# Kernel tuning notes

Hardware: AMD Instinct MI355X
Metric: run time of the kernel (lower is better)

The kernel has to match this reference:

```python
import jax, jax.numpy as jnp
import numpy as np

B, S, D, H = 2, 2048, 1024, 16
DH = D // H  # head dim = 64


def setup_inputs() -> dict:
    key = jax.random.key(0)
    ks = jax.random.split(key, 10)
    q = jax.random.normal(ks[0], (B, S, D), dtype=jnp.float32)
    k = jax.random.normal(ks[1], (B, S, D), dtype=jnp.float32)
    v = jax.random.normal(ks[2], (B, S, D), dtype=jnp.float32)
    # causal mask: True = masked (as in masked_fill)
    causal = jnp.triu(jnp.ones((S, S), dtype=bool), k=1)
    mask = jnp.broadcast_to(causal, (B, S, S))
    sc = 1.0 / np.sqrt(D)
    Wv = jax.random.normal(ks[3], (DH, D), dtype=jnp.float32) * sc
    bv = jnp.zeros((DH,), dtype=jnp.float32)
    Wq = jax.random.normal(ks[4], (H, DH, D), dtype=jnp.float32) * sc  # per-head query proj
    bq = jnp.zeros((H, DH), dtype=jnp.float32)
    Wk = jax.random.normal(ks[5], (H, DH, D), dtype=jnp.float32) * sc  # per-head key proj
    bk = jnp.zeros((H, DH), dtype=jnp.float32)
    Wo = jax.random.normal(ks[6], (D, DH), dtype=jnp.float32) * (1.0 / np.sqrt(DH))  # final proj, no bias
    return {"q": q, "k": k, "v": v, "mask": mask,
            "Wv": Wv, "bv": bv, "Wq": Wq, "bq": bq, "Wk": Wk, "bk": bk, "Wo": Wo}


def reference(q, k, v, mask, Wv, bv, Wq, bq, Wk, bk, Wo):
    # shared value projection across heads: [B,S,DH]
    v_proj = jnp.einsum('bsd,ed->bse', v, Wv) + bv
    # per-head Q/K projections, batched over heads: [B,H,S,DH]
    qh = jnp.einsum('bsd,hed->bhse', q, Wq) + bq[None, :, None, :]
    kh = jnp.einsum('bsd,hed->bhse', k, Wk) + bk[None, :, None, :]
    scale = jnp.sqrt(jnp.asarray(DH, dtype=qh.dtype))
    attn = jnp.einsum('bhse,bhte->bhst', qh, kh) / scale  # [B,H,S,S]
    attn = jnp.where(mask[:, None, :, :], jnp.asarray(-1e9, attn.dtype), attn)
    attn = jax.nn.softmax(attn, axis=-1)
    out_h = jnp.einsum('bhst,bte->bhse', attn, v_proj)  # shared V across heads
    mean_head = out_h.mean(axis=1)  # mean over heads: [B,S,DH]
    out = jnp.einsum('bse,de->bsd', mean_head, Wo)  # [B,S,D]
    attn_stacked = jnp.transpose(attn, (0, 2, 1, 3))  # [B,S,H,S] to match torch.stack(dim=2)
    return out, attn_stacked
```

## Files before the change

### kernel.cpp

```cpp
#include <hip/hip_runtime.h>
#include <cstdint>
#include <math.h>

typedef unsigned short u16;
typedef __bf16 bf16x8 __attribute__((ext_vector_type(8)));
typedef float f32x4 __attribute__((ext_vector_type(4)));

constexpr int Bc = 2, Sc = 2048, Dc = 1024, Hc = 16, DHc = 64;

__device__ __forceinline__ u16 f2bf(float f) {
  uint32_t u = __builtin_bit_cast(uint32_t, f);
  u += 0x7fffu + ((u >> 16) & 1u);
  return (u16)(u >> 16);
}
__device__ __forceinline__ float bf2f(u16 h) {
  uint32_t u = ((uint32_t)h) << 16;
  return __builtin_bit_cast(float, u);
}
__device__ __forceinline__ f32x4 mfma16(bf16x8 a, bf16x8 b, f32x4 c) {
  return __builtin_amdgcn_mfma_f32_16x16x32_bf16(a, b, c, 0, 0, 0);
}
__device__ __forceinline__ void gload16(const void* g, void* l) {
  __builtin_amdgcn_global_load_lds((const uint32_t*)g, (uint32_t*)l, 16, 0, 0);
}
__device__ __forceinline__ bf16x8 pk8(f32x4 a, f32x4 b) {
  alignas(16) u16 t[8];
  #pragma unroll
  for (int j = 0; j < 4; ++j) { t[j] = f2bf(a[j]); t[4 + j] = f2bf(b[j]); }
  return *reinterpret_cast<const bf16x8*>(t);
}

__global__ __launch_bounds__(256) void cvt_all(
    const float* __restrict__ q, const float* __restrict__ k, const float* __restrict__ v,
    const float* __restrict__ Wq, const float* __restrict__ Wk,
    const float* __restrict__ Wv, const float* __restrict__ Wo,
    u16* __restrict__ qo, u16* __restrict__ ko, u16* __restrict__ vo,
    u16* __restrict__ Wqo, u16* __restrict__ Wko, u16* __restrict__ Wvo,
    u16* __restrict__ Woo) {
  constexpr int NQ = Bc * Sc * Dc / 4;
  constexpr int NW = Hc * DHc * Dc / 4;
  constexpr int NS = DHc * Dc / 4;
  constexpr int C1 = NQ, C2 = 2 * NQ, C3 = 3 * NQ;
  constexpr int C4 = C3 + NW, C5 = C4 + NW, C6 = C5 + NS, C7 = C6 + NS;
  const int i = blockIdx.x * 256 + threadIdx.x;
  if (i >= C7) return;
  const float* src; u16* dst; int j;
  if (i < C1)      { src = q;  dst = qo;  j = i; }
  else if (i < C2) { src = k;  dst = ko;  j = i - C1; }
  else if (i < C3) { src = v;  dst = vo;  j = i - C2; }
  else if (i < C4) { src = Wq; dst = Wqo; j = i - C3; }
  else if (i < C5) { src = Wk; dst = Wko; j = i - C4; }
  else if (i < C6) { src = Wv; dst = Wvo; j = i - C5; }
  else             { src = Wo; dst = Woo; j = i - C6; }
  float4 x = reinterpret_cast<const float4*>(src)[j];
  ushort4 o;
  o.x = f2bf(x.x); o.y = f2bf(x.y); o.z = f2bf(x.z); o.w = f2bf(x.w);
  reinterpret_cast<ushort4*>(dst)[j] = o;
}

__global__ __launch_bounds__(256) void gemm_qkv(
    const u16* __restrict__ qbf, const u16* __restrict__ kbf, const u16* __restrict__ vbf,
    const u16* __restrict__ Wqb, const u16* __restrict__ Wkb, const u16* __restrict__ Wvb,
    const float* __restrict__ bq, const float* __restrict__ bk, const float* __restrict__ bv,
    float qscale, u16* __restrict__ qh, u16* __restrict__ kh, u16* __restrict__ vT) {
  constexpr int K = 1024;
  const int z = blockIdx.z;
  if (z == 2 && blockIdx.x != 0) return;
  const u16* A  = z == 0 ? qbf : (z == 1 ? kbf : vbf);
  const u16* Bw = z == 0 ? Wqb : (z == 1 ? Wkb : Wvb);
  const float* bias = z == 0 ? bq : (z == 1 ? bk : bv);
  const float scale = z == 0 ? qscale : 1.0f;

  __shared__ u16 As[128 * 32];
  __shared__ u16 Bs[128 * 32];
  const int tid = threadIdx.x;
  const int lane = tid & 63;
  const int w = tid >> 6, wm = w >> 1, wn = w & 1;
  const int lo = lane & 15, hi = lane >> 4;
  const int m0 = blockIdx.y * 128, n0 = blockIdx.x * 128;
  const int r16 = lane >> 2;
  const int c8 = (lane & 3) * 8;
  const f32x4 vzero = {0.f, 0.f, 0.f, 0.f};

  f32x4 acc[4][4];
  #pragma unroll
  for (int i = 0; i < 4; ++i)
    #pragma unroll
    for (int j = 0; j < 4; ++j) acc[i][j] = vzero;

  for (int k0 = 0; k0 < K; k0 += 32) {
    #pragma unroll
    for (int it = 0; it < 2; ++it) {
      const int rg = w * 2 + it;
      const int row = rg * 16 + r16;
      gload16(&A[(long)(m0 + row) * K + k0 + c8], &As[rg * 512]);
      gload16(&Bw[(long)(n0 + row) * K + k0 + c8], &Bs[rg * 512]);
    }
    __syncthreads();
    bf16x8 af[4], bfr[4];
    #pragma unroll
    for (int mi = 0; mi < 4; ++mi)
      af[mi] = *reinterpret_cast<const bf16x8*>(&As[(wm * 64 + mi * 16 + lo) * 32 + hi * 8]);
    #pragma unroll
    for (int nj = 0; nj < 4; ++nj)
      bfr[nj] = *reinterpret_cast<const bf16x8*>(&Bs[(wn * 64 + nj * 16 + lo) * 32 + hi * 8]);
    #pragma unroll
    for (int mi = 0; mi < 4; ++mi)
      #pragma unroll
      for (int nj = 0; nj < 4; ++nj)
        acc[mi][nj] = mfma16(af[mi], bfr[nj], acc[mi][nj]);
    __syncthreads();
  }

  #pragma unroll
  for (int nj = 0; nj < 4; ++nj) {
    const int n = n0 + wn * 64 + nj * 16 + lo;
    if (z == 2 && n >= 64) continue;
    const float bb = bias[n];
    #pragma unroll
    for (int mi = 0; mi < 4; ++mi) {
      #pragma unroll
      for (int r = 0; r < 4; ++r) {
        const int mm = m0 + wm * 64 + mi * 16 + hi * 4 + r;
        const int bidx = mm >> 11, ss = mm & 2047;
        const float val = (acc[mi][nj][r] + bb) * scale;
        if (z < 2) {
          const int hh = n >> 6, ee = n & 63;
          const long idx = bidx * 2097152L + ss * 64L + hh * 131072L + ee;
          (z ? kh : qh)[idx] = f2bf(val);
        } else {
          vT[bidx * 131072L + n * 2048L + ss] = f2bf(val);
        }
      }
    }
  }
}

__global__ __launch_bounds__(256) void gemm_bt(
    const u16* __restrict__ A, const u16* __restrict__ Bw,
    const float* __restrict__ bias, int M, int N, int K, float scale,
    u16* __restrict__ outb, float* __restrict__ outf,
    int DHn, long strideB, long strideS, long strideH, long strideE) {
  __shared__ u16 As[128 * 32];
  __shared__ u16 Bs[128 * 32];
  const int tid = threadIdx.x;
  const int lane = tid & 63;
  const int w = tid >> 6, wm = w >> 1, wn = w & 1;
  const int lo = lane & 15, hi = lane >> 4;
  const int m0 = blockIdx.y * 128, n0 = blockIdx.x * 128;
  const int r16 = lane >> 2;
  const int c8 = (lane & 3) * 8;
  const f32x4 vzero = {0.f, 0.f, 0.f, 0.f};

  f32x4 acc[4][4];
  #pragma unroll
  for (int i = 0; i < 4; ++i)
    #pragma unroll
    for (int j = 0; j < 4; ++j) acc[i][j] = vzero;

  for (int k0 = 0; k0 < K; k0 += 32) {
    #pragma unroll
    for (int it = 0; it < 2; ++it) {
      const int rg = w * 2 + it;
      const int row = rg * 16 + r16;
      gload16(&A[(long)(m0 + row) * K + k0 + c8], &As[rg * 512]);
      gload16(&Bw[(long)(n0 + row) * K + k0 + c8], &Bs[rg * 512]);
    }
    __syncthreads();
    bf16x8 af[4], bfr[4];
    #pragma unroll
    for (int mi = 0; mi < 4; ++mi)
      af[mi] = *reinterpret_cast<const bf16x8*>(&As[(wm * 64 + mi * 16 + lo) * 32 + hi * 8]);
    #pragma unroll
    for (int nj = 0; nj < 4; ++nj)
      bfr[nj] = *reinterpret_cast<const bf16x8*>(&Bs[(wn * 64 + nj * 16 + lo) * 32 + hi * 8]);
    #pragma unroll
    for (int mi = 0; mi < 4; ++mi)
      #pragma unroll
      for (int nj = 0; nj < 4; ++nj)
        acc[mi][nj] = mfma16(af[mi], bfr[nj], acc[mi][nj]);
    __syncthreads();
  }

  #pragma unroll
  for (int nj = 0; nj < 4; ++nj) {
    const int n = n0 + wn * 64 + nj * 16 + lo;
    if (n >= N) continue;
    const float bb = bias ? bias[n] : 0.f;
    const int hh = n / DHn, ee = n % DHn;
    #pragma unroll
    for (int mi = 0; mi < 4; ++mi) {
      #pragma unroll
      for (int r = 0; r < 4; ++r) {
        const int mm = m0 + wm * 64 + mi * 16 + hi * 4 + r;
        const int bidx = mm >> 11, ss = mm & 2047;
        const long idx = bidx * strideB + ss * strideS + hh * strideH + ee * strideE;
        const float val = (acc[mi][nj][r] + bb) * scale;
        if (outf) outf[idx] = val;
        else outb[idx] = f2bf(val);
      }
    }
  }
}

__global__ __launch_bounds__(256) void attn_fused(
    const u16* __restrict__ qh, const u16* __restrict__ kh,
    const u16* __restrict__ vT, u16* __restrict__ outh,
    float* __restrict__ attn_out) {
  __shared__ float pslds[4][16][68];
  __shared__ float pofflds[4][16];
  const int tid = threadIdx.x;
  const int lane = tid & 63, w = tid >> 6;
  const int lo = lane & 15, hi = lane >> 4;
  const int blk = blockIdx.x;
  const int sb = blk & 15, h = (blk >> 4) & 15, b = blk >> 8;
  const long bh = (long)(b * Hc + h) * Sc;
  const long rowstride = (long)Hc * Sc;
  float* aout = attn_out + (long)b * Sc * rowstride + (long)h * Sc;
  float (*pf)[68] = pslds[w];
  float* poff = pofflds[w];
  const f32x4 vzero = {0.f, 0.f, 0.f, 0.f};
  const int idx = sb * 4 + w;
  const float M0 = 16.f;

  #pragma unroll 1
  for (int sp = 0; sp < 2; ++sp) {
    const int strip = sp ? 127 - idx : idx;
    const int s0 = strip * 16;
    const int smax = s0 + 15;
    const int send = (smax / 64 + 1) * 64;
    const int srow = s0 + hi * 4;
    const int srow2 = s0 + lo;

    bf16x8 qa0, qa1;
    {
      const u16* qp = &qh[(bh + s0 + lo) * DHc];
      qa0 = *reinterpret_cast<const bf16x8*>(&qp[hi * 8]);
      qa1 = *reinterpret_cast<const bf16x8*>(&qp[32 + hi * 8]);
    }

    float lr[4];
    #pragma unroll
    for (int r = 0; r < 4; ++r) lr[r] = 0.f;

    for (int t0 = 0; t0 < send; t0 += 64) {
      f32x4 z[4];
      #pragma unroll
      for (int c = 0; c < 4; ++c) {
        const u16* kp = &kh[(bh + t0 + c * 16 + lo) * DHc];
        bf16x8 kb0 = *reinterpret_cast<const bf16x8*>(&kp[hi * 8]);
        bf16x8 kb1 = *reinterpret_cast<const bf16x8*>(&kp[32 + hi * 8]);
        f32x4 zz = mfma16(qa0, kb0, vzero);
        z[c] = mfma16(qa1, kb1, zz);
      }
      const bool full = (t0 + 63 <= s0);
      #pragma unroll
      for (int r = 0; r < 4; ++r) {
        const int s = srow + r;
        #pragma unroll
        for (int c = 0; c < 4; ++c) {
          float e = exp2f(z[c][r] - M0);
          if (!full) e = ((t0 + c * 16 + lo) <= s) ? e : 0.f;
          lr[r] += e;
        }
      }
    }
    #pragma unroll
    for (int r = 0; r < 4; ++r) {
      #pragma unroll
      for (int dd = 1; dd < 16; dd <<= 1) lr[r] += __shfl_xor(lr[r], dd);
    }
    if (lo == 0) {
      #pragma unroll
      for (int r = 0; r < 4; ++r) poff[hi * 4 + r] = M0 + __log2f(lr[r]);
    }
    asm volatile("s_waitcnt lgkmcnt(0)" ::: "memory");
    __builtin_amdgcn_sched_barrier(0);
    const float offv = poff[lo];

    f32x4 acco[4];
    #pragma unroll
    for (int eb = 0; eb < 4; ++eb) acco[eb] = vzero;
    const int r4 = lane >> 4;
    const int c4 = (lane & 15) * 4;
    for (int t0 = 0; t0 < send; t0 += 64) {
      const bool full = (t0 + 63 <= s0);
      #pragma unroll
      for (int c = 0; c < 4; ++c) {
        const u16* kp = &kh[(bh + t0 + c * 16 + lo) * DHc];
        bf16x8 kb0 = *reinterpret_cast<const bf16x8*>(&kp[hi * 8]);
        bf16x8 kb1 = *reinterpret_cast<const bf16x8*>(&kp[32 + hi * 8]);
        f32x4 zt = mfma16(kb1, qa1, mfma16(kb0, qa0, vzero));
        f32x4 p;
        #pragma unroll
        for (int r = 0; r < 4; ++r) {
          const float e = exp2f(zt[r] - offv);
          p[r] = (full || (t0 + c * 16 + hi * 4 + r <= srow2)) ? e : 0.f;
        }
        *reinterpret_cast<f32x4*>(&pf[lo][c * 16 + hi * 4]) = p;
      }
      asm volatile("s_waitcnt lgkmcnt(0)" ::: "memory");
      __builtin_amdgcn_sched_barrier(0);
      #pragma unroll
      for (int j = 0; j < 4; ++j) {
        f32x4 v = *reinterpret_cast<const f32x4*>(&pf[j * 4 + r4][c4]);
        __builtin_nontemporal_store(
            v, reinterpret_cast<f32x4*>(aout + (long)(s0 + j * 4 + r4) * rowstride + t0 + c4));
      }
      f32x4 a0 = *reinterpret_cast<const f32x4*>(&pf[lo][hi * 8]);
      f32x4 a1 = *reinterpret_cast<const f32x4*>(&pf[lo][hi * 8 + 4]);
      f32x4 a2 = *reinterpret_cast<const f32x4*>(&pf[lo][32 + hi * 8]);
      f32x4 a3 = *reinterpret_cast<const f32x4*>(&pf[lo][32 + hi * 8 + 4]);
      bf16x8 pa0 = pk8(a0, a1);
      bf16x8 pa1 = pk8(a2, a3);
      const u16* vp = &vT[((long)b * DHc + lo) * Sc + t0 + hi * 8];
      #pragma unroll
      for (int eb = 0; eb < 4; ++eb) {
        bf16x8 vb0 = *reinterpret_cast<const bf16x8*>(&vp[(long)eb * 16 * Sc]);
        bf16x8 vb1 = *reinterpret_cast<const bf16x8*>(&vp[(long)eb * 16 * Sc + 32]);
        acco[eb] = mfma16(pa0, vb0, acco[eb]);
        acco[eb] = mfma16(pa1, vb1, acco[eb]);
      }
    }

    #pragma unroll
    for (int eb = 0; eb < 4; ++eb)
      #pragma unroll
      for (int r = 0; r < 4; ++r)
        outh[(bh + srow + r) * DHc + eb * 16 + lo] = f2bf(acco[eb][r]);

    const f32x4 z4 = {0.f, 0.f, 0.f, 0.f};
    for (int t0 = send; t0 < Sc; t0 += 64) {
      #pragma unroll
      for (int r = 0; r < 4; ++r)
        __builtin_nontemporal_store(
            z4, reinterpret_cast<f32x4*>(aout + (long)(srow + r) * rowstride + t0 + lo * 4));
    }
  }
}

__global__ __launch_bounds__(256) void mean_kernel(const u16* __restrict__ outh,
                                                   u16* __restrict__ meanb) {
  const int idx = blockIdx.x * 256 + threadIdx.x;
  const int bs = idx >> 3;
  const int e0 = (idx & 7) * 8;
  const int b = bs >> 11, s = bs & 2047;
  float acc[8];
  #pragma unroll
  for (int j = 0; j < 8; ++j) acc[j] = 0.f;
  for (int h = 0; h < Hc; ++h) {
    alignas(16) u16 tmp[8];
    *reinterpret_cast<uint4*>(tmp) =
        *reinterpret_cast<const uint4*>(&outh[((long)(b * Hc + h) * Sc + s) * DHc + e0]);
    #pragma unroll
    for (int j = 0; j < 8; ++j) acc[j] += bf2f(tmp[j]);
  }
  alignas(16) u16 o[8];
  #pragma unroll
  for (int j = 0; j < 8; ++j) o[j] = f2bf(acc[j] * 0.0625f);
  *reinterpret_cast<uint4*>(&meanb[(long)bs * DHc + e0]) = *reinterpret_cast<const uint4*>(o);
}

extern "C" void kernel_launch(void* const* d_in, const int* in_sizes, int n_in,
                              void* d_out, int out_size, void* d_ws, size_t ws_size,
                              hipStream_t stream) {
  (void)in_sizes; (void)n_in; (void)out_size; (void)ws_size;
  const float* q  = (const float*)d_in[0];
  const float* k  = (const float*)d_in[1];
  const float* v  = (const float*)d_in[2];
  const float* Wv = (const float*)d_in[4];
  const float* bv = (const float*)d_in[5];
  const float* Wq = (const float*)d_in[6];
  const float* bq = (const float*)d_in[7];
  const float* Wk = (const float*)d_in[8];
  const float* bk = (const float*)d_in[9];
  const float* Wo = (const float*)d_in[10];

  char* ws = (char*)d_ws;
  u16* qbf   = (u16*)(ws + 0);
  u16* kbf   = (u16*)(ws + 8388608);
  u16* vbf   = (u16*)(ws + 16777216);
  u16* Wqbf  = (u16*)(ws + 25165824);
  u16* Wkbf  = (u16*)(ws + 27262976);
  u16* Wvbf  = (u16*)(ws + 29360128);
  u16* Wobf  = (u16*)(ws + 29491200);
  u16* qhb   = (u16*)(ws + 29622272);
  u16* khb   = (u16*)(ws + 38010880);
  u16* vTb   = (u16*)(ws + 46399488);
  u16* outh  = (u16*)(ws + 46923776);
  u16* meanb = (u16*)(ws + 55312384);

  float* outp  = (float*)d_out;
  float* attnp = (float*)d_out + (long)Bc * Sc * Dc;

  cvt_all<<<(3702784 + 255) / 256, 256, 0, stream>>>(
      q, k, v, Wq, Wk, Wv, Wo, qbf, kbf, vbf, Wqbf, Wkbf, Wvbf, Wobf);

  const int M = Bc * Sc;
  const float qscale = 0.125f * 1.4426950408889634f;
  gemm_qkv<<<dim3(8, 32, 3), 256, 0, stream>>>(
      qbf, kbf, vbf, Wqbf, Wkbf, Wvbf, bq, bk, bv, qscale, qhb, khb, vTb);

  attn_fused<<<512, 256, 0, stream>>>(qhb, khb, vTb, outh, attnp);

  mean_kernel<<<128, 256, 0, stream>>>(outh, meanb);

  gemm_bt<<<dim3(8, 32), 256, 0, stream>>>(meanb, Wobf, nullptr, M, 1024, 64, 1.0f,
      nullptr, outp, 1024, 2097152L, 1024L, 0L, 1L);
}
```

Measured before the change: 267.4 us.

## Process both causal strips together per wave to share K and V loads

Each wave used to handle its short and long query strips one after the other. It now runs both strips interleaved in a single pair of passes over the keys, so every K tile and V tile loaded from memory serves both strips whenever the short strip is still active. This removes roughly a third of the K/V global loads and the second loop's setup overhead, and adds independent MFMA work to hide latency. The cost is double the LDS scratch and more live registers (two sets of Q fragments, accumulators and K/V fragments), which may reduce occupancy.

```diff
diff --git a/kernel.cpp b/kernel.cpp
--- a/kernel.cpp
+++ b/kernel.cpp
@@ -207,8 +207,8 @@
     const u16* __restrict__ qh, const u16* __restrict__ kh,
     const u16* __restrict__ vT, u16* __restrict__ outh,
     float* __restrict__ attn_out) {
-  __shared__ float pslds[4][16][68];
-  __shared__ float pofflds[4][16];
+  __shared__ float pslds[2][4][16][68];
+  __shared__ float pofflds[2][4][16];
   const int tid = threadIdx.x;
   const int lane = tid & 63, w = tid >> 6;
   const int lo = lane & 15, hi = lane >> 4;
@@ -217,125 +217,203 @@
   const long bh = (long)(b * Hc + h) * Sc;
   const long rowstride = (long)Hc * Sc;
   float* aout = attn_out + (long)b * Sc * rowstride + (long)h * Sc;
-  float (*pf)[68] = pslds[w];
-  float* poff = pofflds[w];
+  float (*pfA)[68] = pslds[0][w];
+  float (*pfB)[68] = pslds[1][w];
+  float* poffA = pofflds[0][w];
+  float* poffB = pofflds[1][w];
   const f32x4 vzero = {0.f, 0.f, 0.f, 0.f};
   const int idx = sb * 4 + w;
   const float M0 = 16.f;
 
-  #pragma unroll 1
-  for (int sp = 0; sp < 2; ++sp) {
-    const int strip = sp ? 127 - idx : idx;
-    const int s0 = strip * 16;
-    const int smax = s0 + 15;
-    const int send = (smax / 64 + 1) * 64;
-    const int srow = s0 + hi * 4;
-    const int srow2 = s0 + lo;
-
-    bf16x8 qa0, qa1;
+  const int s0A = idx * 16;
+  const int s0B = (127 - idx) * 16;
+  const int sendA = (s0A + 79) & ~63;
+  const int sendB = (s0B + 79) & ~63;
+  const int srowA = s0A + hi * 4;
+  const int srowB = s0B + hi * 4;
+  const int srow2A = s0A + lo;
+  const int srow2B = s0B + lo;
+
+  bf16x8 qaA0, qaA1, qaB0, qaB1;
+  {
+    const u16* qpA = &qh[(bh + s0A + lo) * DHc];
+    qaA0 = *reinterpret_cast<const bf16x8*>(&qpA[hi * 8]);
+    qaA1 = *reinterpret_cast<const bf16x8*>(&qpA[32 + hi * 8]);
+    const u16* qpB = &qh[(bh + s0B + lo) * DHc];
+    qaB0 = *reinterpret_cast<const bf16x8*>(&qpB[hi * 8]);
+    qaB1 = *reinterpret_cast<const bf16x8*>(&qpB[32 + hi * 8]);
+  }
+
+  float lrA[4], lrB[4];
+  #pragma unroll
+  for (int r = 0; r < 4; ++r) { lrA[r] = 0.f; lrB[r] = 0.f; }
+
+  for (int t0 = 0; t0 < sendB; t0 += 64) {
+    bf16x8 kb[4][2];
+    #pragma unroll
+    for (int c = 0; c < 4; ++c) {
+      const u16* kp = &kh[(bh + t0 + c * 16 + lo) * DHc];
+      kb[c][0] = *reinterpret_cast<const bf16x8*>(&kp[hi * 8]);
+      kb[c][1] = *reinterpret_cast<const bf16x8*>(&kp[32 + hi * 8]);
+    }
+    const bool doA = (t0 < sendA);
     {
-      const u16* qp = &qh[(bh + s0 + lo) * DHc];
-      qa0 = *reinterpret_cast<const bf16x8*>(&qp[hi * 8]);
-      qa1 = *reinterpret_cast<const bf16x8*>(&qp[32 + hi * 8]);
-    }
-
-    float lr[4];
-    #pragma unroll
-    for (int r = 0; r < 4; ++r) lr[r] = 0.f;
-
-    for (int t0 = 0; t0 < send; t0 += 64) {
-      f32x4 z[4];
+      const bool fullB = (t0 + 63 <= s0B);
       #pragma unroll
       for (int c = 0; c < 4; ++c) {
-        const u16* kp = &kh[(bh + t0 + c * 16 + lo) * DHc];
-        bf16x8 kb0 = *reinterpret_cast<const bf16x8*>(&kp[hi * 8]);
-        bf16x8 kb1 = *reinterpret_cast<const bf16x8*>(&kp[32 + hi * 8]);
-        f32x4 zz = mfma16(qa0, kb0, vzero);
-        z[c] = mfma16(qa1, kb1, zz);
-      }
-      const bool full = (t0 + 63 <= s0);
-      #pragma unroll
-      for (int r = 0; r < 4; ++r) {
-        const int s = srow + r;
+        f32x4 z = mfma16(qaB1, kb[c][1], mfma16(qaB0, kb[c][0], vzero));
         #pragma unroll
-        for (int c = 0; c < 4; ++c) {
-          float e = exp2f(z[c][r] - M0);
-          if (!full) e = ((t0 + c * 16 + lo) <= s) ? e : 0.f;
-          lr[r] += e;
+        for (int r = 0; r < 4; ++r) {
+          float e = exp2f(z[r] - M0);
+          if (!fullB) e = ((t0 + c * 16 + lo) <= srowB + r) ? e : 0.f;
+          lrB[r] += e;
         }
       }
     }
+    if (doA) {
+      const bool fullA = (t0 + 63 <= s0A);
+      #pragma unroll
+      for (int c = 0; c < 4; ++c) {
+        f32x4 z = mfma16(qaA1, kb[c][1], mfma16(qaA0, kb[c][0], vzero));
+        #pragma unroll
+        for (int r = 0; r < 4; ++r) {
+          float e = exp2f(z[r] - M0);
+          if (!fullA) e = ((t0 + c * 16 + lo) <= srowA + r) ? e : 0.f;
+          lrA[r] += e;
+        }
+      }
+    }
+  }
+  #pragma unroll
+  for (int r = 0; r < 4; ++r) {
+    #pragma unroll
+    for (int dd = 1; dd < 16; dd <<= 1) {
+      lrA[r] += __shfl_xor(lrA[r], dd);
+      lrB[r] += __shfl_xor(lrB[r], dd);
+    }
+  }
+  if (lo == 0) {
     #pragma unroll
     for (int r = 0; r < 4; ++r) {
-      #pragma unroll
-      for (int dd = 1; dd < 16; dd <<= 1) lr[r] += __shfl_xor(lr[r], dd);
-    }
-    if (lo == 0) {
-      #pragma unroll
-      for (int r = 0; r < 4; ++r) poff[hi * 4 + r] = M0 + __log2f(lr[r]);
-    }
-    asm volatile("s_waitcnt lgkmcnt(0)" ::: "memory");
-    __builtin_amdgcn_sched_barrier(0);
-    const float offv = poff[lo];
-
-    f32x4 acco[4];
-    #pragma unroll
-    for (int eb = 0; eb < 4; ++eb) acco[eb] = vzero;
-    const int r4 = lane >> 4;
-    const int c4 = (lane & 15) * 4;
-    for (int t0 = 0; t0 < send; t0 += 64) {
-      const bool full = (t0 + 63 <= s0);
+      poffA[hi * 4 + r] = M0 + __log2f(lrA[r]);
+      poffB[hi * 4 + r] = M0 + __log2f(lrB[r]);
+    }
+  }
+  asm volatile("s_waitcnt lgkmcnt(0)" ::: "memory");
+  __builtin_amdgcn_sched_barrier(0);
+  const float offA = poffA[lo];
+  const float offB = poffB[lo];
+
+  f32x4 accoA[4], accoB[4];
+  #pragma unroll
+  for (int eb = 0; eb < 4; ++eb) { accoA[eb] = vzero; accoB[eb] = vzero; }
+  const int r4 = lane >> 4;
+  const int c4 = (lane & 15) * 4;
+
+  for (int t0 = 0; t0 < sendB; t0 += 64) {
+    bf16x8 kb[4][2];
+    #pragma unroll
+    for (int c = 0; c < 4; ++c) {
+      const u16* kp = &kh[(bh + t0 + c * 16 + lo) * DHc];
+      kb[c][0] = *reinterpret_cast<const bf16x8*>(&kp[hi * 8]);
+      kb[c][1] = *reinterpret_cast<const bf16x8*>(&kp[32 + hi * 8]);
+    }
+    const bool doA = (t0 < sendA);
+    {
+      const bool fullB = (t0 + 63 <= s0B);
       #pragma unroll
       for (int c = 0; c < 4; ++c) {
-        const u16* kp = &kh[(bh + t0 + c * 16 + lo) * DHc];
-        bf16x8 kb0 = *reinterpret_cast<const bf16x8*>(&kp[hi * 8]);
-        bf16x8 kb1 = *reinterpret_cast<const bf16x8*>(&kp[32 + hi * 8]);
-        f32x4 zt = mfma16(kb1, qa1, mfma16(kb0, qa0, vzero));
+        f32x4 zt = mfma16(kb[c][1], qaB1, mfma16(kb[c][0], qaB0, vzero));
         f32x4 p;
         #pragma unroll
         for (int r = 0; r < 4; ++r) {
-          const float e = exp2f(zt[r] - offv);
-          p[r] = (full || (t0 + c * 16 + hi * 4 + r <= srow2)) ? e : 0.f;
+          const float e = exp2f(zt[r] - offB);
+          p[r] = (fullB || (t0 + c * 16 + hi * 4 + r <= srow2B)) ? e : 0.f;
         }
-        *reinterpret_cast<f32x4*>(&pf[lo][c * 16 + hi * 4]) = p;
-      }
-      asm volatile("s_waitcnt lgkmcnt(0)" ::: "memory");
-      __builtin_amdgcn_sched_barrier(0);
+        *reinterpret_cast<f32x4*>(&pfB[lo][c * 16 + hi * 4]) = p;
+      }
+    }
+    if (doA) {
+      const bool fullA = (t0 + 63 <= s0A);
+      #pragma unroll
+      for (int c = 0; c < 4; ++c) {
+        f32x4 zt = mfma16(kb[c][1], qaA1, mfma16(kb[c][0], qaA0, vzero));
+        f32x4 p;
+        #pragma unroll
+        for (int r = 0; r < 4; ++r) {
+          const float e = exp2f(zt[r] - offA);
+          p[r] = (fullA || (t0 + c * 16 + hi * 4 + r <= srow2A)) ? e : 0.f;
+        }
+        *reinterpret_cast<f32x4*>(&pfA[lo][c * 16 + hi * 4]) = p;
+      }
+    }
+    asm volatile("s_waitcnt lgkmcnt(0)" ::: "memory");
+    __builtin_amdgcn_sched_barrier(0);
+    #pragma unroll
+    for (int j = 0; j < 4; ++j) {
+      f32x4 v = *reinterpret_cast<const f32x4*>(&pfB[j * 4 + r4][c4]);
+      __builtin_nontemporal_store(
+          v, reinterpret_cast<f32x4*>(aout + (long)(s0B + j * 4 + r4) * rowstride + t0 + c4));
+    }
+    if (doA) {
       #pragma unroll
       for (int j = 0; j < 4; ++j) {
-        f32x4 v = *reinterpret_cast<const f32x4*>(&pf[j * 4 + r4][c4]);
+        f32x4 v = *reinterpret_cast<const f32x4*>(&pfA[j * 4 + r4][c4]);
         __builtin_nontemporal_store(
-            v, reinterpret_cast<f32x4*>(aout + (long)(s0 + j * 4 + r4) * rowstride + t0 + c4));
-      }
-      f32x4 a0 = *reinterpret_cast<const f32x4*>(&pf[lo][hi * 8]);
-      f32x4 a1 = *reinterpret_cast<const f32x4*>(&pf[lo][hi * 8 + 4]);
-      f32x4 a2 = *reinterpret_cast<const f32x4*>(&pf[lo][32 + hi * 8]);
-      f32x4 a3 = *reinterpret_cast<const f32x4*>(&pf[lo][32 + hi * 8 + 4]);
+            v, reinterpret_cast<f32x4*>(aout + (long)(s0A + j * 4 + r4) * rowstride + t0 + c4));
+      }
+    }
+    bf16x8 vb[4][2];
+    const u16* vp = &vT[((long)b * DHc + lo) * Sc + t0 + hi * 8];
+    #pragma unroll
+    for (int eb = 0; eb < 4; ++eb) {
+      vb[eb][0] = *reinterpret_cast<const bf16x8*>(&vp[(long)eb * 16 * Sc]);
+      vb[eb][1] = *reinterpret_cast<const bf16x8*>(&vp[(long)eb * 16 * Sc + 32]);
+    }
+    {
+      f32x4 a0 = *reinterpret_cast<const f32x4*>(&pfB[lo][hi * 8]);
+      f32x4 a1 = *reinterpret_cast<const f32x4*>(&pfB[lo][hi * 8 + 4]);
+      f32x4 a2 = *reinterpret_cast<const f32x4*>(&pfB[lo][32 + hi * 8]);
+      f32x4 a3 = *reinterpret_cast<const f32x4*>(&pfB[lo][32 + hi * 8 + 4]);
       bf16x8 pa0 = pk8(a0, a1);
       bf16x8 pa1 = pk8(a2, a3);
-      const u16* vp = &vT[((long)b * DHc + lo) * Sc + t0 + hi * 8];
-      #pragma unroll
-      for (int eb = 0; eb < 4; ++eb) {
-        bf16x8 vb0 = *reinterpret_cast<const bf16x8*>(&vp[(long)eb * 16 * Sc]);
-        bf16x8 vb1 = *reinterpret_cast<const bf16x8*>(&vp[(long)eb * 16 * Sc + 32]);
-        acco[eb] = mfma16(pa0, vb0, acco[eb]);
-        acco[eb] = mfma16(pa1, vb1, acco[eb]);
-      }
-    }
-
-    #pragma unroll
-    for (int eb = 0; eb < 4; ++eb)
-      #pragma unroll
-      for (int r = 0; r < 4; ++r)
-        outh[(bh + srow + r) * DHc + eb * 16 + lo] = f2bf(acco[eb][r]);
-
-    const f32x4 z4 = {0.f, 0.f, 0.f, 0.f};
-    for (int t0 = send; t0 < Sc; t0 += 64) {
-      #pragma unroll
-      for (int r = 0; r < 4; ++r)
-        __builtin_nontemporal_store(
-            z4, reinterpret_cast<f32x4*>(aout + (long)(srow + r) * rowstride + t0 + lo * 4));
-    }
+      #pragma unroll
+      for (int eb = 0; eb < 4; ++eb)
+        accoB[eb] = mfma16(pa1, vb[eb][1], mfma16(pa0, vb[eb][0], accoB[eb]));
+    }
+    if (doA) {
+      f32x4 a0 = *reinterpret_cast<const f32x4*>(&pfA[lo][hi * 8]);
+      f32x4 a1 = *reinterpret_cast<const f32x4*>(&pfA[lo][hi * 8 + 4]);
+      f32x4 a2 = *reinterpret_cast<const f32x4*>(&pfA[lo][32 + hi * 8]);
+      f32x4 a3 = *reinterpret_cast<const f32x4*>(&pfA[lo][32 + hi * 8 + 4]);
+      bf16x8 pa0 = pk8(a0, a1);
+      bf16x8 pa1 = pk8(a2, a3);
+      #pragma unroll
+      for (int eb = 0; eb < 4; ++eb)
+        accoA[eb] = mfma16(pa1, vb[eb][1], mfma16(pa0, vb[eb][0], accoA[eb]));
+    }
+  }
+
+  #pragma unroll
+  for (int eb = 0; eb < 4; ++eb)
+    #pragma unroll
+    for (int r = 0; r < 4; ++r) {
+      outh[(bh + srowA + r) * DHc + eb * 16 + lo] = f2bf(accoA[eb][r]);
+      outh[(bh + srowB + r) * DHc + eb * 16 + lo] = f2bf(accoB[eb][r]);
+    }
+
+  const f32x4 z4 = {0.f, 0.f, 0.f, 0.f};
+  for (int t0 = sendA; t0 < Sc; t0 += 64) {
+    #pragma unroll
+    for (int r = 0; r < 4; ++r)
+      __builtin_nontemporal_store(
+          z4, reinterpret_cast<f32x4*>(aout + (long)(srowA + r) * rowstride + t0 + lo * 4));
+  }
+  for (int t0 = sendB; t0 < Sc; t0 += 64) {
+    #pragma unroll
+    for (int r = 0; r < 4; ++r)
+      __builtin_nontemporal_store(
+          z4, reinterpret_cast<f32x4*>(aout + (long)(srowB + r) * rowstride + t0 + lo * 4));
   }
 }
 
```

New measurement: 255.8 us. 4.3% less time.
